# Optimization experiments

Hardware: AMD Instinct MI355X
Metric: run time of the kernel (lower is better)

## Reference

```python
import jax, jax.numpy as jnp
import numpy as np

B, N, C, H = 2, 2048, 1024, 16
D = C // H  # head_dim = 64
ROPE_THETA = 500000.0
INIT_STD = 0.02


def setup_inputs() -> dict:
    key = jax.random.key(0)
    ks = jax.random.split(key, 6)
    hidden_states = jax.random.normal(ks[0], (B, N, C), dtype=jnp.float32)
    # rotary embeddings: standard llama-style, built from rope_theta
    inv_freq = jnp.asarray(1.0 / (ROPE_THETA ** (np.arange(0, D, 2, dtype=np.float32) / D)), jnp.float32)
    freqs = jnp.outer(jnp.arange(N, dtype=jnp.float32), inv_freq)  # (N, D/2)
    emb = jnp.concatenate([freqs, freqs], axis=-1)  # (N, D)
    cos = jnp.broadcast_to(jnp.cos(emb)[None], (B, N, D))
    sin = jnp.broadcast_to(jnp.sin(emb)[None], (B, N, D))
    Wq = jax.random.normal(ks[1], (C, C), jnp.float32) * INIT_STD
    Wk = jax.random.normal(ks[2], (C, C), jnp.float32) * INIT_STD
    Wv = jax.random.normal(ks[3], (C, C), jnp.float32) * INIT_STD
    Wo = jax.random.normal(ks[4], (C, C), jnp.float32) * INIT_STD
    return {"hidden_states": hidden_states, "cos": cos, "sin": sin,
            "Wq": Wq, "Wk": Wk, "Wv": Wv, "Wo": Wo}


def _rotate_half(x):
    x1, x2 = x[..., : D // 2], x[..., D // 2 :]
    return jnp.concatenate((-x2, x1), axis=-1)


def reference(hidden_states, cos, sin, Wq, Wk, Wv, Wo):
    scaling = D ** -0.5
    # projections; W stored as (in, out) so y = x @ W
    q = (hidden_states @ Wq) * scaling
    k = hidden_states @ Wk
    v = hidden_states @ Wv
    q = q.reshape(B, N, H, D)
    k = k.reshape(B, N, H, D)
    v = v.reshape(B, N, H, D)
    # RoPE, cos/sin broadcast over heads: (B,N,1,D)
    c = cos[:, :, None, :]
    s = sin[:, :, None, :]
    q = q * c + _rotate_half(q) * s
    k = k * c + _rotate_half(k) * s
    # causal SDPA (q already scaled)
    scores = jnp.einsum("bqhd,bkhd->bhqk", q, k)  # (B,H,N,N)
    causal = jnp.tril(jnp.ones((N, N), dtype=bool))
    scores = jnp.where(causal[None, None], scores, jnp.finfo(scores.dtype).min)
    probs = jax.nn.softmax(scores, axis=-1)
    out = jnp.einsum("bhqk,bkhd->bqhd", probs, v).reshape(B, N, C)
    return out @ Wo
```

## Files before the change

kernel.cpp:

```cpp
#include <hip/hip_runtime.h>
#include <hip/hip_bf16.h>

typedef __hip_bfloat16 bf16;
typedef __attribute__((ext_vector_type(8))) short short8;
typedef __attribute__((ext_vector_type(4))) short short4v;
typedef __attribute__((ext_vector_type(4))) float f32x4;

#define BB 2
#define NN 2048
#define CC 1024
#define HH 16
#define DD 64
#define MM (BB*NN)
#define QKVN 3072
#define LOG2E 1.44269504088896340736f

__device__ __forceinline__ void glds16(const void* g, void* l) {
    __builtin_amdgcn_global_load_lds((const __attribute__((address_space(1))) void*)g,
                                     (__attribute__((address_space(3))) void*)l, 16, 0, 0);
}
__device__ __forceinline__ short pkbf(float x) { bf16 t = (bf16)x; return *(short*)&t; }
__device__ __forceinline__ float b2f(short s) {
    return __uint_as_float(((unsigned)(unsigned short)s) << 16);
}

__global__ __launch_bounds__(256) void convert_f32_bf16(const float* __restrict__ in,
                                                        bf16* __restrict__ out) {
    int i = blockIdx.x * 256 + threadIdx.x;
    float4 v = ((const float4*)in)[i];
    short4v s;
    s.x = pkbf(v.x); s.y = pkbf(v.y); s.z = pkbf(v.z); s.w = pkbf(v.w);
    *((short4v*)out + i) = s;
}

__global__ __launch_bounds__(256) void transpose4(const float* __restrict__ W0,
                                                  const float* __restrict__ W1,
                                                  const float* __restrict__ W2,
                                                  const float* __restrict__ W3,
                                                  bf16* __restrict__ Wtqkv,
                                                  bf16* __restrict__ Wto) {
    __shared__ float t[32][33];
    const int z = blockIdx.z;
    const float* W = z == 0 ? W0 : (z == 1 ? W1 : (z == 2 ? W2 : W3));
    bf16* dst = z < 3 ? Wtqkv + (size_t)z * CC * CC : Wto;
    const int tx = threadIdx.x, ty = threadIdx.y;
    const int x0 = blockIdx.x * 32, y0 = blockIdx.y * 32;
    #pragma unroll
    for (int i = 0; i < 4; ++i)
        t[ty + i * 8][tx] = W[(size_t)(y0 + ty + i * 8) * CC + x0 + tx];
    __syncthreads();
    #pragma unroll
    for (int i = 0; i < 4; ++i)
        dst[(size_t)(x0 + ty + i * 8) * CC + y0 + tx] = (bf16)t[tx][ty + i * 8];
}

template<int Nn, int MODE>
__global__ __launch_bounds__(256) void gemm3(const bf16* __restrict__ A,
                                             const bf16* __restrict__ Bt,
                                             void* __restrict__ Cout,
                                             const float* __restrict__ cosp,
                                             const float* __restrict__ sinp,
                                             bf16* __restrict__ VtOut) {
    __shared__ __align__(16) bf16 As[2][128 * 32];
    __shared__ __align__(16) bf16 Bs[2][128 * 32];
    const int tid = threadIdx.x, lane = tid & 63, wid = tid >> 6;
    const int wr = wid >> 1, wc = wid & 1, l16 = lane & 15, lg = lane >> 4;
    const int n0 = blockIdx.x * 128, m0 = blockIdx.y * 128;

    f32x4 acc[4][4];
    #pragma unroll
    for (int i = 0; i < 4; ++i)
        #pragma unroll
        for (int j = 0; j < 4; ++j) acc[i][j] = {0.f, 0.f, 0.f, 0.f};

    const int issue0 = wid * 2;
    const int sr0 = (issue0 * 1024 + lane * 16) >> 6;
    const int sc0 = ((issue0 * 1024 + lane * 16) & 63) >> 1;
    const int sr1 = ((issue0 + 1) * 1024 + lane * 16) >> 6;
    const int sc1 = (((issue0 + 1) * 1024 + lane * 16) & 63) >> 1;

    auto stage = [&](int k0, int bufi) {
        glds16(&A [(size_t)(m0 + sr0) * 1024 + k0 + sc0], (char*)&As[bufi][0] + issue0 * 1024);
        glds16(&Bt[(size_t)(n0 + sr0) * 1024 + k0 + sc0], (char*)&Bs[bufi][0] + issue0 * 1024);
        glds16(&A [(size_t)(m0 + sr1) * 1024 + k0 + sc1], (char*)&As[bufi][0] + (issue0 + 1) * 1024);
        glds16(&Bt[(size_t)(n0 + sr1) * 1024 + k0 + sc1], (char*)&Bs[bufi][0] + (issue0 + 1) * 1024);
    };

    stage(0, 0);
    for (int t = 0; t < 32; ++t) {
        const int cur = t & 1;
        __syncthreads();
        if (t + 1 < 32) stage((t + 1) * 32, cur ^ 1);
        short8 af[4], bfr[4];
        #pragma unroll
        for (int i = 0; i < 4; ++i) af[i]  = *(const short8*)((char*)&As[cur][0] + (wr * 64 + i * 16 + l16) * 64 + lg * 16);
        #pragma unroll
        for (int j = 0; j < 4; ++j) bfr[j] = *(const short8*)((char*)&Bs[cur][0] + (wc * 64 + j * 16 + l16) * 64 + lg * 16);
        #pragma unroll
        for (int i = 0; i < 4; ++i)
            #pragma unroll
            for (int j = 0; j < 4; ++j)
                acc[i][j] = __builtin_amdgcn_mfma_f32_16x16x32_bf16(af[i], bfr[j], acc[i][j], 0, 0, 0);
    }

    if (MODE == 1 && n0 >= 2 * CC) {
        #pragma unroll
        for (int i = 0; i < 4; ++i) {
            const int row0 = m0 + wr * 64 + i * 16 + lg * 4;
            const int bb = row0 >> 11, nn_ = row0 & (NN - 1);
            #pragma unroll
            for (int j = 0; j < 4; ++j) {
                const int col = n0 - 2 * CC + wc * 64 + j * 16 + l16;
                const int hh = col >> 6, d = col & 63;
                short4v s4;
                #pragma unroll
                for (int r = 0; r < 4; ++r) s4[r] = pkbf(acc[i][j][r]);
                *(short4v*)&VtOut[((size_t)(bb * HH + hh) * DD + d) * NN + nn_] = s4;
            }
        }
    } else if (MODE == 1) {
        const float qs = (n0 < CC) ? 0.125f * LOG2E : 1.0f;
        bf16* Cb = (bf16*)Cout;
        #pragma unroll
        for (int i = 0; i < 4; ++i)
            #pragma unroll
            for (int r = 0; r < 4; ++r) {
                const int row = m0 + wr * 64 + i * 16 + lg * 4 + r;
                #pragma unroll
                for (int j = 0; j < 2; ++j) {
                    const int d = j * 16 + l16;
                    const float cv = cosp[(size_t)row * DD + d];
                    const float sv = sinp[(size_t)row * DD + d];
                    const float x1 = acc[i][j][r];
                    const float x2 = acc[i][j + 2][r];
                    const size_t cbase = (size_t)row * QKVN + n0 + wc * 64 + j * 16 + l16;
                    Cb[cbase]      = (bf16)((x1 * cv - x2 * sv) * qs);
                    Cb[cbase + 32] = (bf16)((x2 * cv + x1 * sv) * qs);
                }
            }
    } else {
        float* Cf = (float*)Cout;
        #pragma unroll
        for (int i = 0; i < 4; ++i)
            #pragma unroll
            for (int r = 0; r < 4; ++r) {
                const int row = m0 + wr * 64 + i * 16 + lg * 4 + r;
                #pragma unroll
                for (int j = 0; j < 4; ++j)
                    Cf[(size_t)row * Nn + n0 + wc * 64 + j * 16 + l16] = acc[i][j][r];
            }
    }
}

__global__ __launch_bounds__(256) void flash_mfma4(const bf16* __restrict__ QKV,
                                                   const bf16* __restrict__ Vt,
                                                   bf16* __restrict__ PartA,
                                                   bf16* __restrict__ PartB,
                                                   float2* __restrict__ Mlb) {
    __shared__ __align__(16) bf16 Ks[2][4096];
    __shared__ __align__(16) bf16 Vs[2][4096];
    const int tid = threadIdx.x, lane = tid & 63, wid = tid >> 6;
    const int l16 = lane & 15, lg = lane >> 4;
    const int bid = blockIdx.x;
    const int bh = bid & 31;
    const int slot = bid >> 5;
    const int qt = 31 - (slot >> 1);
    const int half = slot & 1;
    const int h = bh & (HH - 1), b = bh >> 4;
    const int wq0 = qt * 64 + wid * 16;
    const int nkt = qt + 1;
    const int hf = (nkt + 1) >> 1;
    const int t0 = half ? hf : 0;
    const int cnt = (half ? nkt : hf) - t0;
    const int grow = b * NN + wq0 + l16;

    const bf16* Kbase = QKV + (size_t)b * NN * QKVN + CC + h * DD;
    const bf16* Vbase = Vt + (size_t)(b * HH + h) * DD * NN;

    short8 qf[2];
    #pragma unroll
    for (int ch = 0; ch < 2; ++ch)
        qf[ch] = *(const short8*)&QKV[(size_t)grow * QKVN + h * DD + ch * 32 + lg * 8];

    f32x4 o[4];
    #pragma unroll
    for (int dn = 0; dn < 4; ++dn) o[dn] = {0.f, 0.f, 0.f, 0.f};
    float mx = -1e30f, ls = 0.f;

    const int a0 = (wid * 2) * 1024 + lane * 16, a1 = a0 + 1024;
    const int r0 = a0 >> 7, c0 = ((a0 & 127) ^ ((r0 & 7) << 4)) >> 1;
    const int r1 = a1 >> 7, c1 = ((a1 & 127) ^ ((r1 & 7) << 4)) >> 1;
    const bf16* kp0 = Kbase + (size_t)(t0 * 64 + r0) * QKVN + c0;
    const bf16* kp1 = Kbase + (size_t)(t0 * 64 + r1) * QKVN + c1;
    const bf16* vp0 = Vbase + (size_t)r0 * NN + t0 * 64 + c0;
    const bf16* vp1 = Vbase + (size_t)r1 * NN + t0 * 64 + c1;
    char* ldsK = (char*)&Ks[0][0] + wid * 2048;
    char* ldsV = (char*)&Vs[0][0] + wid * 2048;

    auto stage = [&](int par) {
        glds16(kp0, ldsK + par * 8192);
        glds16(kp1, ldsK + par * 8192 + 1024);
        glds16(vp0, ldsV + par * 8192);
        glds16(vp1, ldsV + par * 8192 + 1024);
        kp0 += 64 * QKVN; kp1 += 64 * QKVN; vp0 += 64; vp1 += 64;
    };

    if (cnt > 0) stage(0);
    for (int i = 0; i < cnt; ++i) {
        __syncthreads();
        if (i + 1 < cnt) stage((i + 1) & 1);
        const int cur = i & 1;
        const int kt = t0 + i;
        const int k0 = kt * 64;

        f32x4 st[4];
        #pragma unroll
        for (int kc = 0; kc < 4; ++kc) st[kc] = {0.f, 0.f, 0.f, 0.f};
        __builtin_amdgcn_s_setprio(1);
        #pragma unroll
        for (int kc = 0; kc < 4; ++kc) {
            const int row = kc * 16 + l16;
            const char* rb = (const char*)&Ks[cur][0] + row * 128;
            const int sw = (row & 7) << 4;
            short8 kf0 = *(const short8*)(rb + ((lg * 16) ^ sw));
            short8 kf1 = *(const short8*)(rb + ((64 + lg * 16) ^ sw));
            st[kc] = __builtin_amdgcn_mfma_f32_16x16x32_bf16(kf0, qf[0], st[kc], 0, 0, 0);
            st[kc] = __builtin_amdgcn_mfma_f32_16x16x32_bf16(kf1, qf[1], st[kc], 0, 0, 0);
        }
        __builtin_amdgcn_s_setprio(0);

        if (kt == qt) {
            #pragma unroll
            for (int kc = 0; kc < 4; ++kc)
                #pragma unroll
                for (int r = 0; r < 4; ++r)
                    if (k0 + kc * 16 + lg * 4 + r > wq0 + l16) st[kc][r] = -1e30f;
        }

        float rm = fmaxf(fmaxf(st[0][0], st[0][1]), fmaxf(st[0][2], st[0][3]));
        #pragma unroll
        for (int kc = 1; kc < 4; ++kc)
            rm = fmaxf(rm, fmaxf(fmaxf(st[kc][0], st[kc][1]), fmaxf(st[kc][2], st[kc][3])));
        rm = fmaxf(rm, __shfl_xor(rm, 16, 64));
        rm = fmaxf(rm, __shfl_xor(rm, 32, 64));
        if (__any(rm > mx + 8.0f)) {
            const float mn = fmaxf(mx, rm);
            const float sc = __builtin_amdgcn_exp2f(mx - mn);
            ls *= sc;
            #pragma unroll
            for (int dn = 0; dn < 4; ++dn) {
                o[dn][0] *= sc; o[dn][1] *= sc; o[dn][2] *= sc; o[dn][3] *= sc;
            }
            mx = mn;
        }
        float rs = 0.f;
        #pragma unroll
        for (int kc = 0; kc < 4; ++kc)
            #pragma unroll
            for (int r = 0; r < 4; ++r) {
                const float p = __builtin_amdgcn_exp2f(st[kc][r] - mx);
                st[kc][r] = p; rs += p;
            }
        rs += __shfl_xor(rs, 16, 64);
        rs += __shfl_xor(rs, 32, 64);
        ls += rs;

        __builtin_amdgcn_s_setprio(1);
        #pragma unroll
        for (int kc = 0; kc < 4; ++kc) {
            short4v pf;
            pf[0] = pkbf(st[kc][0]); pf[1] = pkbf(st[kc][1]);
            pf[2] = pkbf(st[kc][2]); pf[3] = pkbf(st[kc][3]);
            #pragma unroll
            for (int dn = 0; dn < 4; ++dn) {
                const int row = dn * 16 + l16;
                short4v vf = *(const short4v*)((const char*)&Vs[cur][0] + row * 128
                                               + ((kc * 32 + lg * 8) ^ ((row & 7) << 4)));
                o[dn] = __builtin_amdgcn_mfma_f32_16x16x16bf16_1k(vf, pf, o[dn], 0, 0, 0);
            }
        }
        __builtin_amdgcn_s_setprio(0);
    }

    if (lg == 0) Mlb[((size_t)(half * MM) + grow) * HH + h] = make_float2(mx, ls);
    bf16* dst = half ? PartB : PartA;
    const size_t rowb = (size_t)grow * CC + h * DD;
    #pragma unroll
    for (int dn = 0; dn < 4; ++dn) {
        short4v s4;
        s4[0] = pkbf(o[dn][0]); s4[1] = pkbf(o[dn][1]);
        s4[2] = pkbf(o[dn][2]); s4[3] = pkbf(o[dn][3]);
        *(short4v*)&dst[rowb + dn * 16 + lg * 4] = s4;
    }
}

__global__ __launch_bounds__(256) void merge_halves(const bf16* __restrict__ pa,
                                                    const bf16* __restrict__ pb,
                                                    const float2* __restrict__ ml,
                                                    bf16* __restrict__ outp) {
    const int idx = blockIdx.x * 256 + threadIdx.x;
    const int row = idx >> 7;
    const int h = (idx & 127) >> 3;
    const float2 a = ml[(size_t)row * HH + h];
    const float2 bb = ml[((size_t)MM + row) * HH + h];
    const float M = fmaxf(a.x, bb.x);
    const float w0 = __builtin_amdgcn_exp2f(a.x - M);
    const float w1 = (bb.y > 0.f) ? __builtin_amdgcn_exp2f(bb.x - M) : 0.f;
    const float inv = 1.f / (a.y * w0 + bb.y * w1);
    const float f0 = w0 * inv, f1 = w1 * inv;
    const size_t off = (size_t)idx * 8;
    short8 va = *(const short8*)(pa + off);
    short8 vb = *(const short8*)(pb + off);
    short8 ov;
    #pragma unroll
    for (int e = 0; e < 8; ++e)
        ov[e] = pkbf(b2f(va[e]) * f0 + b2f(vb[e]) * f1);
    *(short8*)(outp + off) = ov;
}

extern "C" void kernel_launch(void* const* d_in, const int* in_sizes, int n_in,
                              void* d_out, int out_size, void* d_ws, size_t ws_size,
                              hipStream_t stream) {
    const float* hs   = (const float*)d_in[0];
    const float* cosp = (const float*)d_in[1];
    const float* sinp = (const float*)d_in[2];
    const float* Wq   = (const float*)d_in[3];
    const float* Wk   = (const float*)d_in[4];
    const float* Wv   = (const float*)d_in[5];
    const float* Wo   = (const float*)d_in[6];
    float* out = (float*)d_out;

    char* ws = (char*)d_ws;
    bf16* hsb   = (bf16*)(ws);
    bf16* Wtqkv = (bf16*)(ws + (8  << 20));
    bf16* Wto   = (bf16*)(ws + (14 << 20));
    bf16* QKV   = (bf16*)(ws + (16 << 20));
    bf16* Vtb   = (bf16*)(ws + (40 << 20));
    bf16* Abuf  = hsb;
    float2* Mlb = (float2*)Wtqkv;
    bf16* PartB = (bf16*)out;

    convert_f32_bf16<<<MM * CC / 1024, 256, 0, stream>>>(hs, hsb);

    transpose4<<<dim3(32, 32, 4), dim3(32, 8), 0, stream>>>(Wq, Wk, Wv, Wo, Wtqkv, Wto);

    gemm3<QKVN, 1><<<dim3(QKVN / 128, MM / 128), 256, 0, stream>>>(
        hsb, Wtqkv, QKV, cosp, sinp, Vtb);

    flash_mfma4<<<2048, 256, 0, stream>>>(QKV, Vtb, Abuf, PartB, Mlb);

    merge_halves<<<2048, 256, 0, stream>>>(Abuf, PartB, Mlb, Abuf);

    gemm3<CC, 2><<<dim3(CC / 128, MM / 128), 256, 0, stream>>>(
        Abuf, Wto, out, nullptr, nullptr, nullptr);
}
```

Measured before the change: 129.3 us.

## Use 256x256 ping-pong QKV GEMM and split flash attention into thirds

```diff
diff --git a/kernel.cpp b/kernel.cpp
--- a/kernel.cpp
+++ b/kernel.cpp
@@ -54,13 +54,149 @@
         dst[(size_t)(x0 + ty + i * 8) * CC + y0 + tx] = (bf16)t[tx][ty + i * 8];
 }
 
-template<int Nn, int MODE>
-__global__ __launch_bounds__(256) void gemm3(const bf16* __restrict__ A,
-                                             const bf16* __restrict__ Bt,
-                                             void* __restrict__ Cout,
-                                             const float* __restrict__ cosp,
-                                             const float* __restrict__ sinp,
-                                             bf16* __restrict__ VtOut) {
+__global__ __launch_bounds__(512, 2) void gemm8(const bf16* __restrict__ A,
+                                                const bf16* __restrict__ Bt,
+                                                bf16* __restrict__ Cb,
+                                                const float* __restrict__ cosp,
+                                                const float* __restrict__ sinp,
+                                                bf16* __restrict__ VtOut) {
+    __shared__ __align__(16) bf16 As[2][256 * 64];
+    __shared__ __align__(16) bf16 Bs[2][256 * 64];
+    const int tid = threadIdx.x, lane = tid & 63, wid = tid >> 6;
+    const int wm = wid >> 2, wn = wid & 3, l16 = lane & 15, lg = lane >> 4;
+    const int n0 = blockIdx.x * 256, m0 = blockIdx.y * 256;
+
+    f32x4 acc[8][4];
+    #pragma unroll
+    for (int i = 0; i < 8; ++i)
+        #pragma unroll
+        for (int j = 0; j < 4; ++j) acc[i][j] = {0.f, 0.f, 0.f, 0.f};
+
+    const int srow = lane >> 3;
+    const int sce  = (((lane & 7) * 16) ^ ((lane >> 3) << 4)) >> 1;
+    auto stA = [&](int t, int hf, int bi) {
+        #pragma unroll
+        for (int j = 0; j < 2; ++j) {
+            const int rl = hf * 128 + (wid * 2 + j) * 8;
+            glds16(&A[(size_t)(m0 + rl + srow) * 1024 + t * 64 + sce], (void*)&As[bi][rl * 64]);
+        }
+    };
+    auto stB = [&](int t, int hf, int bi) {
+        #pragma unroll
+        for (int j = 0; j < 2; ++j) {
+            const int rl = hf * 128 + (wid * 2 + j) * 8;
+            glds16(&Bt[(size_t)(n0 + rl + srow) * 1024 + t * 64 + sce], (void*)&Bs[bi][rl * 64]);
+        }
+    };
+
+    short8 af[4][2], bfr[4][2];
+    const int swz = (l16 & 7) << 4;
+    auto rdA = [&](int mh, int bi) {
+        #pragma unroll
+        for (int f = 0; f < 4; ++f) {
+            const char* rb = (const char*)&As[bi][0] + (wm * 128 + (mh * 4 + f) * 16 + l16) * 128;
+            af[f][0] = *(const short8*)(rb + ((lg * 16) ^ swz));
+            af[f][1] = *(const short8*)(rb + ((64 + lg * 16) ^ swz));
+        }
+    };
+    auto rdB = [&](int nh, int bi) {
+        #pragma unroll
+        for (int f = 0; f < 2; ++f) {
+            const char* rb = (const char*)&Bs[bi][0] + (wn * 64 + (nh * 2 + f) * 16 + l16) * 128;
+            bfr[nh * 2 + f][0] = *(const short8*)(rb + ((lg * 16) ^ swz));
+            bfr[nh * 2 + f][1] = *(const short8*)(rb + ((64 + lg * 16) ^ swz));
+        }
+    };
+    auto MF = [&](int mh, int nh) {
+        __builtin_amdgcn_s_setprio(1);
+        #pragma unroll
+        for (int f = 0; f < 4; ++f)
+            #pragma unroll
+            for (int g = 0; g < 2; ++g)
+                #pragma unroll
+                for (int ck = 0; ck < 2; ++ck)
+                    acc[mh * 4 + f][nh * 2 + g] = __builtin_amdgcn_mfma_f32_16x16x32_bf16(
+                        af[f][ck], bfr[nh * 2 + g][ck], acc[mh * 4 + f][nh * 2 + g], 0, 0, 0);
+        __builtin_amdgcn_s_setprio(0);
+    };
+    #define BAR8()   do { __builtin_amdgcn_s_barrier(); __builtin_amdgcn_sched_barrier(0); } while (0)
+    #define LGKM0()  do { asm volatile("s_waitcnt lgkmcnt(0)" ::: "memory"); __builtin_amdgcn_sched_barrier(0); } while (0)
+    #define VM6()    do { asm volatile("s_waitcnt vmcnt(6)" ::: "memory"); __builtin_amdgcn_sched_barrier(0); } while (0)
+
+    stB(0, 0, 0); stB(0, 1, 0); stA(0, 0, 0); stA(0, 1, 0);
+    stB(1, 0, 1); stB(1, 1, 1); stA(1, 0, 1);
+    VM6();
+    BAR8();
+
+    for (int i = 0; i < 8; ++i) {
+        const bool st = (i < 7);
+        rdA(0, 0); rdB(0, 0);
+        stA(2 * i + 1, 1, 1);
+        BAR8(); LGKM0(); MF(0, 0); BAR8();
+        rdB(1, 0);
+        BAR8(); LGKM0(); MF(0, 1); BAR8();
+        rdA(1, 0);
+        if (st) stB(2 * i + 2, 0, 0);
+        BAR8(); LGKM0(); MF(1, 0); BAR8();
+        if (st) { stB(2 * i + 2, 1, 0); stA(2 * i + 2, 0, 0); }
+        BAR8(); LGKM0(); MF(1, 1);
+        VM6(); BAR8();
+        rdA(0, 1); rdB(0, 1);
+        if (st) stA(2 * i + 2, 1, 0);
+        BAR8(); LGKM0(); MF(0, 0); BAR8();
+        rdB(1, 1);
+        BAR8(); LGKM0(); MF(0, 1); BAR8();
+        rdA(1, 1);
+        if (st) stB(2 * i + 3, 0, 1);
+        BAR8(); LGKM0(); MF(1, 0); BAR8();
+        if (st) { stB(2 * i + 3, 1, 1); stA(2 * i + 3, 0, 1); }
+        BAR8(); LGKM0(); MF(1, 1);
+        VM6(); BAR8();
+    }
+    #undef BAR8
+    #undef LGKM0
+    #undef VM6
+
+    if (n0 >= 2 * CC) {
+        #pragma unroll
+        for (int fm = 0; fm < 8; ++fm) {
+            const int row0 = m0 + wm * 128 + fm * 16 + lg * 4;
+            const int bb = row0 >> 11, nn_ = row0 & (NN - 1);
+            #pragma unroll
+            for (int fn = 0; fn < 4; ++fn) {
+                const int col = n0 - 2 * CC + wn * 64 + fn * 16 + l16;
+                const int hh = col >> 6, d = col & 63;
+                short4v s4;
+                #pragma unroll
+                for (int r = 0; r < 4; ++r) s4[r] = pkbf(acc[fm][fn][r]);
+                *(short4v*)&VtOut[((size_t)(bb * HH + hh) * DD + d) * NN + nn_] = s4;
+            }
+        }
+    } else {
+        const float qs = (n0 < CC) ? 0.125f * LOG2E : 1.0f;
+        #pragma unroll
+        for (int fm = 0; fm < 8; ++fm)
+            #pragma unroll
+            for (int r = 0; r < 4; ++r) {
+                const int row = m0 + wm * 128 + fm * 16 + lg * 4 + r;
+                #pragma unroll
+                for (int j = 0; j < 2; ++j) {
+                    const int d = j * 16 + l16;
+                    const float cv = cosp[(size_t)row * DD + d];
+                    const float sv = sinp[(size_t)row * DD + d];
+                    const float x1 = acc[fm][j][r];
+                    const float x2 = acc[fm][j + 2][r];
+                    const size_t cbase = (size_t)row * QKVN + n0 + wn * 64 + j * 16 + l16;
+                    Cb[cbase]      = (bf16)((x1 * cv - x2 * sv) * qs);
+                    Cb[cbase + 32] = (bf16)((x2 * cv + x1 * sv) * qs);
+                }
+            }
+    }
+}
+
+__global__ __launch_bounds__(256) void gemm3o(const bf16* __restrict__ A,
+                                              const bf16* __restrict__ Bt,
+                                              float* __restrict__ Cf) {
     __shared__ __align__(16) bf16 As[2][128 * 32];
     __shared__ __align__(16) bf16 Bs[2][128 * 32];
     const int tid = threadIdx.x, lane = tid & 63, wid = tid >> 6;
@@ -103,59 +239,22 @@
                 acc[i][j] = __builtin_amdgcn_mfma_f32_16x16x32_bf16(af[i], bfr[j], acc[i][j], 0, 0, 0);
     }
 
-    if (MODE == 1 && n0 >= 2 * CC) {
-        #pragma unroll
-        for (int i = 0; i < 4; ++i) {
-            const int row0 = m0 + wr * 64 + i * 16 + lg * 4;
-            const int bb = row0 >> 11, nn_ = row0 & (NN - 1);
-            #pragma unroll
-            for (int j = 0; j < 4; ++j) {
-                const int col = n0 - 2 * CC + wc * 64 + j * 16 + l16;
-                const int hh = col >> 6, d = col & 63;
-                short4v s4;
-                #pragma unroll
-                for (int r = 0; r < 4; ++r) s4[r] = pkbf(acc[i][j][r]);
-                *(short4v*)&VtOut[((size_t)(bb * HH + hh) * DD + d) * NN + nn_] = s4;
-            }
-        }
-    } else if (MODE == 1) {
-        const float qs = (n0 < CC) ? 0.125f * LOG2E : 1.0f;
-        bf16* Cb = (bf16*)Cout;
-        #pragma unroll
-        for (int i = 0; i < 4; ++i)
-            #pragma unroll
-            for (int r = 0; r < 4; ++r) {
-                const int row = m0 + wr * 64 + i * 16 + lg * 4 + r;
-                #pragma unroll
-                for (int j = 0; j < 2; ++j) {
-                    const int d = j * 16 + l16;
-                    const float cv = cosp[(size_t)row * DD + d];
-                    const float sv = sinp[(size_t)row * DD + d];
-                    const float x1 = acc[i][j][r];
-                    const float x2 = acc[i][j + 2][r];
-                    const size_t cbase = (size_t)row * QKVN + n0 + wc * 64 + j * 16 + l16;
-                    Cb[cbase]      = (bf16)((x1 * cv - x2 * sv) * qs);
-                    Cb[cbase + 32] = (bf16)((x2 * cv + x1 * sv) * qs);
-                }
-            }
-    } else {
-        float* Cf = (float*)Cout;
-        #pragma unroll
-        for (int i = 0; i < 4; ++i)
-            #pragma unroll
-            for (int r = 0; r < 4; ++r) {
-                const int row = m0 + wr * 64 + i * 16 + lg * 4 + r;
-                #pragma unroll
-                for (int j = 0; j < 4; ++j)
-                    Cf[(size_t)row * Nn + n0 + wc * 64 + j * 16 + l16] = acc[i][j][r];
-            }
-    }
-}
-
-__global__ __launch_bounds__(256) void flash_mfma4(const bf16* __restrict__ QKV,
+    #pragma unroll
+    for (int i = 0; i < 4; ++i)
+        #pragma unroll
+        for (int r = 0; r < 4; ++r) {
+            const int row = m0 + wr * 64 + i * 16 + lg * 4 + r;
+            #pragma unroll
+            for (int j = 0; j < 4; ++j)
+                Cf[(size_t)row * CC + n0 + wc * 64 + j * 16 + l16] = acc[i][j][r];
+        }
+}
+
+__global__ __launch_bounds__(256) void flash_mfma5(const bf16* __restrict__ QKV,
                                                    const bf16* __restrict__ Vt,
                                                    bf16* __restrict__ PartA,
                                                    bf16* __restrict__ PartB,
+                                                   bf16* __restrict__ PartC,
                                                    float2* __restrict__ Mlb) {
     __shared__ __align__(16) bf16 Ks[2][4096];
     __shared__ __align__(16) bf16 Vs[2][4096];
@@ -164,14 +263,13 @@
     const int bid = blockIdx.x;
     const int bh = bid & 31;
     const int slot = bid >> 5;
-    const int qt = 31 - (slot >> 1);
-    const int half = slot & 1;
+    const int qt = 31 - slot / 3;
+    const int part = slot % 3;
     const int h = bh & (HH - 1), b = bh >> 4;
     const int wq0 = qt * 64 + wid * 16;
     const int nkt = qt + 1;
-    const int hf = (nkt + 1) >> 1;
-    const int t0 = half ? hf : 0;
-    const int cnt = (half ? nkt : hf) - t0;
+    const int t0 = (part * nkt) / 3;
+    const int cnt = ((part + 1) * nkt) / 3 - t0;
     const int grow = b * NN + wq0 + l16;
 
     const bf16* Kbase = QKV + (size_t)b * NN * QKVN + CC + h * DD;
@@ -282,8 +380,8 @@
         __builtin_amdgcn_s_setprio(0);
     }
 
-    if (lg == 0) Mlb[((size_t)(half * MM) + grow) * HH + h] = make_float2(mx, ls);
-    bf16* dst = half ? PartB : PartA;
+    if (lg == 0) Mlb[((size_t)(part * MM) + grow) * HH + h] = make_float2(mx, ls);
+    bf16* dst = part == 0 ? PartA : (part == 1 ? PartB : PartC);
     const size_t rowb = (size_t)grow * CC + h * DD;
     #pragma unroll
     for (int dn = 0; dn < 4; ++dn) {
@@ -294,27 +392,31 @@
     }
 }
 
-__global__ __launch_bounds__(256) void merge_halves(const bf16* __restrict__ pa,
-                                                    const bf16* __restrict__ pb,
-                                                    const float2* __restrict__ ml,
-                                                    bf16* __restrict__ outp) {
+__global__ __launch_bounds__(256) void merge3(const bf16* __restrict__ pa,
+                                              const bf16* __restrict__ pb,
+                                              const bf16* __restrict__ pc,
+                                              const float2* __restrict__ ml,
+                                              bf16* __restrict__ outp) {
     const int idx = blockIdx.x * 256 + threadIdx.x;
     const int row = idx >> 7;
     const int h = (idx & 127) >> 3;
-    const float2 a = ml[(size_t)row * HH + h];
-    const float2 bb = ml[((size_t)MM + row) * HH + h];
-    const float M = fmaxf(a.x, bb.x);
-    const float w0 = __builtin_amdgcn_exp2f(a.x - M);
-    const float w1 = (bb.y > 0.f) ? __builtin_amdgcn_exp2f(bb.x - M) : 0.f;
-    const float inv = 1.f / (a.y * w0 + bb.y * w1);
-    const float f0 = w0 * inv, f1 = w1 * inv;
+    const float2 a  = ml[(size_t)row * HH + h];
+    const float2 b_ = ml[((size_t)MM + row) * HH + h];
+    const float2 c  = ml[((size_t)2 * MM + row) * HH + h];
+    const float M = fmaxf(fmaxf(a.x, b_.x), c.x);
+    const float w0 = (a.y  > 0.f) ? __builtin_amdgcn_exp2f(a.x  - M) : 0.f;
+    const float w1 = (b_.y > 0.f) ? __builtin_amdgcn_exp2f(b_.x - M) : 0.f;
+    const float w2 = (c.y  > 0.f) ? __builtin_amdgcn_exp2f(c.x  - M) : 0.f;
+    const float inv = 1.f / (a.y * w0 + b_.y * w1 + c.y * w2);
+    const float f0 = w0 * inv, f1 = w1 * inv, f2 = w2 * inv;
     const size_t off = (size_t)idx * 8;
     short8 va = *(const short8*)(pa + off);
     short8 vb = *(const short8*)(pb + off);
+    short8 vc = *(const short8*)(pc + off);
     short8 ov;
     #pragma unroll
     for (int e = 0; e < 8; ++e)
-        ov[e] = pkbf(b2f(va[e]) * f0 + b2f(vb[e]) * f1);
+        ov[e] = pkbf(b2f(va[e]) * f0 + b2f(vb[e]) * f1 + b2f(vc[e]) * f2);
     *(short8*)(outp + off) = ov;
 }
 
@@ -339,18 +441,18 @@
     bf16* Abuf  = hsb;
     float2* Mlb = (float2*)Wtqkv;
     bf16* PartB = (bf16*)out;
+    bf16* PartC = (bf16*)out + (size_t)MM * CC;
 
     convert_f32_bf16<<<MM * CC / 1024, 256, 0, stream>>>(hs, hsb);
 
     transpose4<<<dim3(32, 32, 4), dim3(32, 8), 0, stream>>>(Wq, Wk, Wv, Wo, Wtqkv, Wto);
 
-    gemm3<QKVN, 1><<<dim3(QKVN / 128, MM / 128), 256, 0, stream>>>(
+    gemm8<<<dim3(QKVN / 256, MM / 256), 512, 0, stream>>>(
         hsb, Wtqkv, QKV, cosp, sinp, Vtb);
 
-    flash_mfma4<<<2048, 256, 0, stream>>>(QKV, Vtb, Abuf, PartB, Mlb);
-
-    merge_halves<<<2048, 256, 0, stream>>>(Abuf, PartB, Mlb, Abuf);
-
-    gemm3<CC, 2><<<dim3(CC / 128, MM / 128), 256, 0, stream>>>(
-        Abuf, Wto, out, nullptr, nullptr, nullptr);
-}
+    flash_mfma5<<<3072, 256, 0, stream>>>(QKV, Vtb, Abuf, PartB, PartC, Mlb);
+
+    merge3<<<2048, 256, 0, stream>>>(Abuf, PartB, PartC, Mlb, Abuf);
+
+    gemm3o<<<dim3(CC / 128, MM / 128), 256, 0, stream>>>(Abuf, Wto, out);
+}
```

Result: no change. 127.0 us (-1.8%).

## Split causal flash attention KV range three ways and defer row-sum shuffles

Applied to the files above, without the earlier changes.

```diff
diff --git a/kernel.cpp b/kernel.cpp
--- a/kernel.cpp
+++ b/kernel.cpp
@@ -152,10 +152,11 @@
     }
 }
 
-__global__ __launch_bounds__(256) void flash_mfma4(const bf16* __restrict__ QKV,
+__global__ __launch_bounds__(256) void flash_mfma6(const bf16* __restrict__ QKV,
                                                    const bf16* __restrict__ Vt,
                                                    bf16* __restrict__ PartA,
                                                    bf16* __restrict__ PartB,
+                                                   bf16* __restrict__ PartC,
                                                    float2* __restrict__ Mlb) {
     __shared__ __align__(16) bf16 Ks[2][4096];
     __shared__ __align__(16) bf16 Vs[2][4096];
@@ -164,14 +165,13 @@
     const int bid = blockIdx.x;
     const int bh = bid & 31;
     const int slot = bid >> 5;
-    const int qt = 31 - (slot >> 1);
-    const int half = slot & 1;
+    const int qt = 31 - slot / 3;
+    const int part = slot % 3;
     const int h = bh & (HH - 1), b = bh >> 4;
     const int wq0 = qt * 64 + wid * 16;
     const int nkt = qt + 1;
-    const int hf = (nkt + 1) >> 1;
-    const int t0 = half ? hf : 0;
-    const int cnt = (half ? nkt : hf) - t0;
+    const int t0 = (part * nkt) / 3;
+    const int cnt = ((part + 1) * nkt) / 3 - t0;
     const int grow = b * NN + wq0 + l16;
 
     const bf16* Kbase = QKV + (size_t)b * NN * QKVN + CC + h * DD;
@@ -241,10 +241,10 @@
         #pragma unroll
         for (int kc = 1; kc < 4; ++kc)
             rm = fmaxf(rm, fmaxf(fmaxf(st[kc][0], st[kc][1]), fmaxf(st[kc][2], st[kc][3])));
-        rm = fmaxf(rm, __shfl_xor(rm, 16, 64));
-        rm = fmaxf(rm, __shfl_xor(rm, 32, 64));
         if (__any(rm > mx + 8.0f)) {
-            const float mn = fmaxf(mx, rm);
+            float wmx = fmaxf(rm, __shfl_xor(rm, 16, 64));
+            wmx = fmaxf(wmx, __shfl_xor(wmx, 32, 64));
+            const float mn = fmaxf(mx, wmx);
             const float sc = __builtin_amdgcn_exp2f(mx - mn);
             ls *= sc;
             #pragma unroll
@@ -261,8 +261,6 @@
                 const float p = __builtin_amdgcn_exp2f(st[kc][r] - mx);
                 st[kc][r] = p; rs += p;
             }
-        rs += __shfl_xor(rs, 16, 64);
-        rs += __shfl_xor(rs, 32, 64);
         ls += rs;
 
         __builtin_amdgcn_s_setprio(1);
@@ -282,8 +280,10 @@
         __builtin_amdgcn_s_setprio(0);
     }
 
-    if (lg == 0) Mlb[((size_t)(half * MM) + grow) * HH + h] = make_float2(mx, ls);
-    bf16* dst = half ? PartB : PartA;
+    ls += __shfl_xor(ls, 16, 64);
+    ls += __shfl_xor(ls, 32, 64);
+    if (lg == 0) Mlb[((size_t)(part * MM) + grow) * HH + h] = make_float2(mx, ls);
+    bf16* dst = part == 0 ? PartA : (part == 1 ? PartB : PartC);
     const size_t rowb = (size_t)grow * CC + h * DD;
     #pragma unroll
     for (int dn = 0; dn < 4; ++dn) {
@@ -294,27 +294,31 @@
     }
 }
 
-__global__ __launch_bounds__(256) void merge_halves(const bf16* __restrict__ pa,
-                                                    const bf16* __restrict__ pb,
-                                                    const float2* __restrict__ ml,
-                                                    bf16* __restrict__ outp) {
+__global__ __launch_bounds__(256) void merge3(const bf16* __restrict__ pa,
+                                              const bf16* __restrict__ pb,
+                                              const bf16* __restrict__ pc,
+                                              const float2* __restrict__ ml,
+                                              bf16* __restrict__ outp) {
     const int idx = blockIdx.x * 256 + threadIdx.x;
     const int row = idx >> 7;
     const int h = (idx & 127) >> 3;
-    const float2 a = ml[(size_t)row * HH + h];
-    const float2 bb = ml[((size_t)MM + row) * HH + h];
-    const float M = fmaxf(a.x, bb.x);
-    const float w0 = __builtin_amdgcn_exp2f(a.x - M);
-    const float w1 = (bb.y > 0.f) ? __builtin_amdgcn_exp2f(bb.x - M) : 0.f;
-    const float inv = 1.f / (a.y * w0 + bb.y * w1);
-    const float f0 = w0 * inv, f1 = w1 * inv;
+    const float2 a  = ml[(size_t)row * HH + h];
+    const float2 b_ = ml[((size_t)MM + row) * HH + h];
+    const float2 c  = ml[((size_t)2 * MM + row) * HH + h];
+    const float M = fmaxf(fmaxf(a.x, b_.x), c.x);
+    const float w0 = (a.y  > 0.f) ? __builtin_amdgcn_exp2f(a.x  - M) : 0.f;
+    const float w1 = (b_.y > 0.f) ? __builtin_amdgcn_exp2f(b_.x - M) : 0.f;
+    const float w2 = (c.y  > 0.f) ? __builtin_amdgcn_exp2f(c.x  - M) : 0.f;
+    const float inv = 1.f / (a.y * w0 + b_.y * w1 + c.y * w2);
+    const float f0 = w0 * inv, f1 = w1 * inv, f2 = w2 * inv;
     const size_t off = (size_t)idx * 8;
     short8 va = *(const short8*)(pa + off);
     short8 vb = *(const short8*)(pb + off);
+    short8 vc = *(const short8*)(pc + off);
     short8 ov;
     #pragma unroll
     for (int e = 0; e < 8; ++e)
-        ov[e] = pkbf(b2f(va[e]) * f0 + b2f(vb[e]) * f1);
+        ov[e] = pkbf(b2f(va[e]) * f0 + b2f(vb[e]) * f1 + b2f(vc[e]) * f2);
     *(short8*)(outp + off) = ov;
 }
 
@@ -339,6 +343,7 @@
     bf16* Abuf  = hsb;
     float2* Mlb = (float2*)Wtqkv;
     bf16* PartB = (bf16*)out;
+    bf16* PartC = (bf16*)out + (size_t)MM * CC;
 
     convert_f32_bf16<<<MM * CC / 1024, 256, 0, stream>>>(hs, hsb);
 
@@ -347,9 +352,9 @@
     gemm3<QKVN, 1><<<dim3(QKVN / 128, MM / 128), 256, 0, stream>>>(
         hsb, Wtqkv, QKV, cosp, sinp, Vtb);
 
-    flash_mfma4<<<2048, 256, 0, stream>>>(QKV, Vtb, Abuf, PartB, Mlb);
-
-    merge_halves<<<2048, 256, 0, stream>>>(Abuf, PartB, Mlb, Abuf);
+    flash_mfma6<<<3072, 256, 0, stream>>>(QKV, Vtb, Abuf, PartB, PartC, Mlb);
+
+    merge3<<<2048, 256, 0, stream>>>(Abuf, PartB, PartC, Mlb, Abuf);
 
     gemm3<CC, 2><<<dim3(CC / 128, MM / 128), 256, 0, stream>>>(
         Abuf, Wto, out, nullptr, nullptr, nullptr);
```

Measured after the change: 127.5 us. No clear change (-1.4%).
